# Kernel tuning notes

Measured on AMD Instinct MI355X. Metric: run time of the kernel, lower is better.

The kernel has to match this reference:

```python
import jax, jax.numpy as jnp
import numpy as np
from math import sqrt

ROPE_BASE = 6000.0


def _rope_tables(seq_len, rope_dim, dtype):
    # inv_freq: [rope_dim/2]; emb = concat(freqs, freqs) along last dim -> [seq_len, rope_dim]
    inv_freq = 1.0 / (ROPE_BASE ** (jnp.arange(0, rope_dim, 2, dtype=jnp.float32) / rope_dim))
    t = jnp.arange(seq_len, dtype=jnp.float32)
    freqs = jnp.outer(t, inv_freq)
    emb = jnp.concatenate([freqs, freqs], axis=-1)
    return jnp.cos(emb).astype(dtype), jnp.sin(emb).astype(dtype)


def _rotate_half(x):
    x1, x2 = jnp.split(x, 2, axis=-1)
    return jnp.concatenate([-x2, x1], axis=-1)


def setup_inputs() -> dict:
    key = jax.random.key(0)
    k1, k2, k3 = jax.random.split(key, 3)
    B, S, D = 2, 2048, 1024
    H, DK = 16, 64
    x = jax.random.normal(k1, (B, S, D), dtype=jnp.float32)
    W_qkv = jax.random.normal(k2, (3, H, DK, D), dtype=jnp.float32) * 0.02
    W_o = jax.random.normal(k3, (D, H * DK), dtype=jnp.float32) * 0.02
    return {"x": x, "W_qkv": W_qkv, "W_o": W_o}


def reference(x, W_qkv, W_o):
    B, S, D = x.shape
    _, H, DK, _ = W_qkv.shape
    rope_dim = DK // 2  # RotaryEmbeddings(dim=d_k // 2)

    # fused QKV projection: [B, 3, H, S, DK]
    qkv = jnp.einsum('bsm,qhdm->bqhsd', x, W_qkv)

    # inline RoPE on Q and K, first rope_dim channels only
    cos, sin = _rope_tables(S, rope_dim, x.dtype)  # [S, rope_dim]
    qk = qkv[:, :2, :, :, :rope_dim]
    qk_rot = qk * cos + _rotate_half(qk) * sin
    qkv = qkv.at[:, :2, :, :, :rope_dim].set(qk_rot)

    Q, K, V = qkv[:, 0], qkv[:, 1], qkv[:, 2]  # [B, H, S, DK]

    scores = jnp.einsum('bhqd,bhkd->bhqk', Q, K)
    causal = jnp.triu(jnp.ones((S, S), dtype=bool), k=1)
    scores = jnp.where(causal, -jnp.inf, scores) / sqrt(DK)
    attn = jax.nn.softmax(scores, axis=-1)
    out = jnp.einsum('bhqk,bhkd->bhqd', attn, V)

    # concat heads: [B, S, H*DK], then output projection (Linear weight [D, H*DK])
    out = out.transpose(0, 2, 1, 3).reshape(B, S, H * DK)
    return jnp.einsum('bsh,dh->bsd', out, W_o)
```

## Files before the change

kernel.cpp:

```cpp
#include <hip/hip_runtime.h>
#include <math.h>


static constexpr int Bb  = 2;
static constexpr int Ss  = 2048;
static constexpr int Hh  = 16;
static constexpr int DKk = 64;

static constexpr size_t QSZ = (size_t)Bb * Hh * Ss * DKk;

static constexpr size_t WOB_E  = 0;
static constexpr size_t XB_E   = 1048576;
static constexpr size_t WQKV_E = 5242880;
static constexpr size_t QB_E   = 9437184;
static constexpr size_t OB_E   = QB_E + 3*QSZ;

typedef __attribute__((ext_vector_type(8))) short short8;
typedef __attribute__((ext_vector_type(4))) float f32x4;

__device__ __forceinline__ unsigned short f2bf(float f) {
    unsigned int u = __float_as_uint(f);
    u += 0x7fffu + ((u >> 16) & 1u);
    return (unsigned short)(u >> 16);
}

__device__ __forceinline__ unsigned int cvtpk_bf16(float lo, float hi) {
    unsigned int r;
    asm("v_cvt_pk_bf16_f32 %0, %1, %2" : "=v"(r) : "v"(lo), "v"(hi));
    return r;
}

__device__ __forceinline__ float fexp2(float x) {
    float r;
    asm("v_exp_f32 %0, %1" : "=v"(r) : "v"(x));
    return r;
}

__device__ __forceinline__ float fsin_rev(float r) {
    float o;
    asm("v_sin_f32 %0, %1" : "=v"(o) : "v"(r));
    return o;
}
__device__ __forceinline__ float fcos_rev(float r) {
    float o;
    asm("v_cos_f32 %0, %1" : "=v"(o) : "v"(r));
    return o;
}

__device__ __forceinline__ void gl16(const unsigned short* g, unsigned short* l) {
    __builtin_amdgcn_global_load_lds(
        (const __attribute__((address_space(1))) void*)g,
        (__attribute__((address_space(3))) void*)l, 16, 0, 0);
}

__global__ __launch_bounds__(256)
void convert_bf16(const float* __restrict__ x, const float* __restrict__ wqkv,
                  const float* __restrict__ wo, unsigned short* __restrict__ dst)
{
    const size_t i4 = ((size_t)blockIdx.x * 256 + threadIdx.x) * 4;
    const float* src;
    if (i4 < 1048576)      src = wo   + i4;
    else if (i4 < 5242880) src = x    + (i4 - 1048576);
    else                   src = wqkv + (i4 - 5242880);
    const float4 v = *(const float4*)src;
    ushort4 p = { f2bf(v.x), f2bf(v.y), f2bf(v.z), f2bf(v.w) };
    *(ushort4*)(dst + i4) = p;
}

template<int MODE, int BN>
__global__ __launch_bounds__(256)
void gemm_mfma(const unsigned short* __restrict__ A,
               const unsigned short* __restrict__ Bm,
               float* __restrict__ C, unsigned short* __restrict__ QKV, int N)
{
    constexpr int K   = 1024;
    constexpr int NF  = BN / 32;
    constexpr int ASZ = 128 * 32;
    constexpr int BSZ = BN * 32;
    __shared__ unsigned short ShPool[2 * ASZ + 2 * BSZ];
    unsigned short* As0 = ShPool;
    unsigned short* As1 = ShPool + ASZ;
    unsigned short* Bs0 = ShPool + 2 * ASZ;
    unsigned short* Bs1 = ShPool + 2 * ASZ + BSZ;

    const int t    = threadIdx.x;
    const int lane = t & 63;
    const int w    = t >> 6;
    const int l15  = lane & 15;
    const int quad = lane >> 4;
    const int wr   = w >> 1;
    const int wc   = w & 1;
    const int n0   = blockIdx.x * BN;
    const int m0   = blockIdx.y * 128;

    const unsigned short* Ag = A  + (size_t)(m0 + (t >> 2)) * K + (t & 3) * 8;
    const unsigned short* Bg = Bm + (size_t)(n0 + (t >> 2)) * K + (t & 3) * 8;

    f32x4 acc[4][NF];
    #pragma unroll
    for (int i = 0; i < 4; i++)
        #pragma unroll
        for (int j = 0; j < NF; j++) acc[i][j] = f32x4{0.f, 0.f, 0.f, 0.f};

    auto stage = [&](int k0, unsigned short* Asb, unsigned short* Bsb) {
        gl16(Ag + k0,        Asb + t*8);
        gl16(Ag + 64*K + k0, Asb + 2048 + t*8);
        gl16(Bg + k0,        Bsb + t*8);
        if (BN == 128) gl16(Bg + 64*K + k0, Bsb + 2048 + t*8);
    };
    auto comp = [&](const unsigned short* Asb, const unsigned short* Bsb) {
        short8 af[4], bfv[NF];
        #pragma unroll
        for (int mf = 0; mf < 4; mf++)
            af[mf] = *(const short8*)&Asb[(wr*64 + mf*16 + l15) * 32 + quad*8];
        #pragma unroll
        for (int nf = 0; nf < NF; nf++)
            bfv[nf] = *(const short8*)&Bsb[(wc*(BN/2) + nf*16 + l15) * 32 + quad*8];
        #pragma unroll
        for (int mf = 0; mf < 4; mf++)
            #pragma unroll
            for (int nf = 0; nf < NF; nf++)
                acc[mf][nf] = __builtin_amdgcn_mfma_f32_16x16x32_bf16(
                    af[mf], bfv[nf], acc[mf][nf], 0, 0, 0);
    };

    stage(0, As0, Bs0);
    for (int k0 = 0; k0 < K; k0 += 64) {
        __syncthreads();
        stage(k0 + 32, As1, Bs1);
        comp(As0, Bs0);
        __syncthreads();
        if (k0 + 64 < K) stage(k0 + 64, As0, Bs0);
        comp(As1, Bs1);
    }

    if (MODE == 0) {
        #pragma unroll
        for (int mf = 0; mf < 4; mf++)
            #pragma unroll
            for (int r = 0; r < 4; r++) {
                float* crow = C + (size_t)(m0 + wr*64 + mf*16 + quad*4 + r) * N
                            + n0 + wc*(BN/2);
                #pragma unroll
                for (int nf = 0; nf < NF; nf++)
                    crow[nf*16 + l15] = acc[mf][nf][r];
            }
    } else {
        __syncthreads();
        const int col0 = n0 + wc*64;
        const int q    = col0 >> 10;
        const int h    = (col0 >> 6) & 15;
        const int row0 = m0 + wr*64;
        const int b    = row0 >> 11;
        const int s0   = row0 & 2047;
        if (q == 2) {
            unsigned short* chunk = ShPool + w * 2048;
            unsigned short* vb = QKV + 2*QSZ
                               + (size_t)(b*Hh + h) * DKk * Ss + s0;
            #pragma unroll
            for (int pass = 0; pass < 2; pass++) {
                #pragma unroll
                for (int mf = 0; mf < 4; mf++)
                    #pragma unroll
                    for (int nfp = 0; nfp < 2; nfp++) {
                        const int nf = pass*2 + nfp;
                        const int dl = nfp*16 + l15;
                        const int sby = (mf*16 + quad*4) * 2;
                        ushort4 pv = { f2bf(acc[mf][nf][0]), f2bf(acc[mf][nf][1]),
                                       f2bf(acc[mf][nf][2]), f2bf(acc[mf][nf][3]) };
                        *(ushort4*)((char*)chunk
                            + dl*128 + (sby ^ ((dl & 7) << 4))) = pv;
                    }
                #pragma unroll
                for (int dblk = 0; dblk < 8; dblk++) {
                    const int dl = dblk*4 + quad;
                    const int sl = l15*4;
                    const ushort4 pv = *(const ushort4*)((char*)chunk
                        + dl*128 + ((sl*2) ^ ((dl & 7) << 4)));
                    *(ushort4*)(vb + (size_t)(pass*32 + dl) * Ss + sl) = pv;
                }
            }
        } else {
            const float qsc = (q == 0) ? 0.125f * 1.44269504088896f : 1.0f;
            const float rev_freq = (float)(exp(-(double)(2 * l15) / 32.0
                                   * log(6000.0)) / 6.283185307179586);
            unsigned short* base = QKV + (size_t)q * QSZ
                                 + ((size_t)(b*Hh + h) * Ss) * DKk;
            #pragma unroll
            for (int mf = 0; mf < 4; mf++)
                #pragma unroll
                for (int r = 0; r < 4; r++) {
                    const int s = s0 + mf*16 + quad*4 + r;
                    float rev = (float)s * rev_freq;
                    rev -= floorf(rev);
                    const float sn = fsin_rev(rev);
                    const float cs = fcos_rev(rev);
                    const float v0 = acc[mf][0][r] * qsc;
                    const float v1 = acc[mf][1][r] * qsc;
                    unsigned short* rowp = base + (size_t)s * DKk;
                    rowp[l15]      = f2bf(v0 * cs - v1 * sn);
                    rowp[16 + l15] = f2bf(v1 * cs + v0 * sn);
                    rowp[32 + l15] = f2bf(acc[mf][2][r] * qsc);
                    rowp[48 + l15] = f2bf(acc[mf][3][r] * qsc);
                }
        }
    }
}

__global__ __launch_bounds__(256)
void flash_mfma(const unsigned short* __restrict__ Qa,
                const unsigned short* __restrict__ Ka,
                const unsigned short* __restrict__ Va,
                unsigned short* __restrict__ Ob)
{
    __shared__ unsigned short Ks0[64*64];
    __shared__ unsigned short Ks1[64*64];
    __shared__ unsigned short Vs0[64*64];
    __shared__ unsigned short Vs1[64*64];

    const int t    = threadIdx.x;
    const int lane = t & 63;
    const int w    = t >> 6;
    const int l15  = lane & 15;
    const int quad = lane >> 4;

    const int bid   = blockIdx.x;
    const int xcd   = bid & 7;
    const int slot  = bid >> 3;
    const bool hv   = slot < 32;
    const int sub   = hv ? slot : slot - 32;
    const int bh    = xcd*4 + (sub >> 3);
    const int j     = sub & 7;
    const int QT    = hv ? 15 - j : j;
    const int n     = 2*QT + 2;

    const int c0 = t,       r0 = c0 >> 3, g0 = ((c0 & 7) ^ (r0 & 7)) * 8;
    const int c1 = t + 256, r1 = c1 >> 3, g1 = ((c1 & 7) ^ (r1 & 7)) * 8;

    auto stage = [&](int skt, unsigned short* Ksb, unsigned short* Vsb) {
        const unsigned short* Kg = Ka + (size_t)bh * Ss * DKk + (size_t)skt*64*DKk;
        const unsigned short* Vg = Va + (size_t)bh * DKk * Ss + skt*64;
        gl16(Kg + (size_t)r0*DKk + g0, Ksb + t*8);
        gl16(Kg + (size_t)r1*DKk + g1, Ksb + (t+256)*8);
        gl16(Vg + (size_t)r0*Ss  + g0, Vsb + t*8);
        gl16(Vg + (size_t)r1*Ss  + g1, Vsb + (t+256)*8);
    };

    short8 qf[2][2];
    f32x4 o[2][4];
    float lacc[2];
    #pragma unroll
    for (int mfq = 0; mfq < 2; mfq++) {
        lacc[mfq] = 0.f;
        #pragma unroll
        for (int i = 0; i < 4; i++) o[mfq][i] = f32x4{0.f,0.f,0.f,0.f};
    }
    #pragma unroll
    for (int mfq = 0; mfq < 2; mfq++) {
        const unsigned short* qrow = Qa + (size_t)bh * Ss * DKk
            + (size_t)(QT*128 + w*32 + mfq*16 + l15) * DKk;
        qf[mfq][0] = *(const short8*)(qrow + quad*8);
        qf[mfq][1] = *(const short8*)(qrow + 32 + quad*8);
    }

    auto compute = [&](const unsigned short* Ksb, const unsigned short* Vsb,
                       int ckt) {
        f32x4 sc[4][2];
        #pragma unroll
        for (int nt = 0; nt < 4; nt++)
            #pragma unroll
            for (int mfq = 0; mfq < 2; mfq++) sc[nt][mfq] = f32x4{0.f,0.f,0.f,0.f};
        #pragma unroll
        for (int nt = 0; nt < 4; nt++)
            #pragma unroll
            for (int kc = 0; kc < 2; kc++) {
                const short8 kf = *(const short8*)&Ksb[(nt*16 + l15)*64
                                   + (((kc*4 + quad) ^ (l15 & 7)) * 8)];
                sc[nt][0] = __builtin_amdgcn_mfma_f32_16x16x32_bf16(kf, qf[0][kc], sc[nt][0], 0,0,0);
                sc[nt][1] = __builtin_amdgcn_mfma_f32_16x16x32_bf16(kf, qf[1][kc], sc[nt][1], 0,0,0);
            }

        if (ckt >= 2*QT) {
            const int kb = ckt*64 + quad*4;
            const int qb = QT*128 + w*32 + l15;
            #pragma unroll
            for (int nt = 0; nt < 4; nt++)
                #pragma unroll
                for (int mfq = 0; mfq < 2; mfq++)
                    #pragma unroll
                    for (int r = 0; r < 4; r++)
                        if (kb + nt*16 + r > qb + mfq*16)
                            sc[nt][mfq][r] = -INFINITY;
        }

        #pragma unroll
        for (int nt = 0; nt < 4; nt++)
            #pragma unroll
            for (int mfq = 0; mfq < 2; mfq++)
                #pragma unroll
                for (int r = 0; r < 4; r++)
                    sc[nt][mfq][r] = fexp2(sc[nt][mfq][r]);
        #pragma unroll
        for (int mfq = 0; mfq < 2; mfq++)
            #pragma unroll
            for (int nt = 0; nt < 4; nt++)
                lacc[mfq] += (sc[nt][mfq][0] + sc[nt][mfq][1])
                           + (sc[nt][mfq][2] + sc[nt][mfq][3]);

        short8 pfrag[2][2];
        #pragma unroll
        for (int mfq = 0; mfq < 2; mfq++)
            #pragma unroll
            for (int kc = 0; kc < 2; kc++) {
                unsigned int pk[4];
                #pragma unroll
                for (int v = 0; v < 4; v++) {
                    const int nt = 2*kc + (v >> 1);
                    const int rr = 2*(v & 1);
                    pk[v] = cvtpk_bf16(sc[nt][mfq][rr], sc[nt][mfq][rr+1]);
                }
                pfrag[mfq][kc] = *(short8*)&pk[0];
            }

        #pragma unroll
        for (int dt = 0; dt < 4; dt++) {
            const int row = dt*16 + l15;
            const int rx  = row & 7;
            const int wi  = 4*(quad & 1);
            #pragma unroll
            for (int kc = 0; kc < 2; kc++) {
                const ushort4 lo = *(const ushort4*)&Vsb[row*64
                                    + (((4*kc + (quad>>1)) ^ rx) * 8) + wi];
                const ushort4 hi = *(const ushort4*)&Vsb[row*64
                                    + (((4*kc + 2 + (quad>>1)) ^ rx) * 8) + wi];
                short8 vf;
                vf[0]=lo.x; vf[1]=lo.y; vf[2]=lo.z; vf[3]=lo.w;
                vf[4]=hi.x; vf[5]=hi.y; vf[6]=hi.z; vf[7]=hi.w;
                o[0][dt] = __builtin_amdgcn_mfma_f32_16x16x32_bf16(
                    pfrag[0][kc], vf, o[0][dt], 0,0,0);
                o[1][dt] = __builtin_amdgcn_mfma_f32_16x16x32_bf16(
                    pfrag[1][kc], vf, o[1][dt], 0,0,0);
            }
        }
    };

    stage(0, Ks0, Vs0);
    int i = 0;
    while (true) {
        __syncthreads();
        const bool h1 = (i + 1 < n);
        if (h1) stage(i + 1, Ks1, Vs1);
        compute(Ks0, Vs0, i);
        if (!h1) break;
        i++;
        __syncthreads();
        const bool h2 = (i + 1 < n);
        if (h2) stage(i + 1, Ks0, Vs0);
        compute(Ks1, Vs1, i);
        if (!h2) break;
        i++;
    }

    {
        const int b = bh >> 4, h = bh & 15;
        const int q0 = QT*128 + w*32;
        #pragma unroll
        for (int mfq = 0; mfq < 2; mfq++) {
            float ls = lacc[mfq];
            ls += __shfl_xor(ls, 16);
            ls += __shfl_xor(ls, 32);
            #pragma unroll
            for (int r = 0; r < 4; r++) {
                const int x = quad*4 + r;
                const float inv = 1.0f / __shfl(ls, (lane & 48) + x);
                const int row = q0 + mfq*16 + x;
                unsigned short* orow = Ob + ((size_t)b*Ss + row) * 1024 + h*64;
                #pragma unroll
                for (int dt = 0; dt < 4; dt++)
                    orow[dt*16 + l15] = f2bf(o[mfq][dt][r] * inv);
            }
        }
    }
}

extern "C" void kernel_launch(void* const* d_in, const int* in_sizes, int n_in,
                              void* d_out, int out_size, void* d_ws, size_t ws_size,
                              hipStream_t stream)
{
    const float* x    = (const float*)d_in[0];
    const float* Wqkv = (const float*)d_in[1];
    const float* Wo   = (const float*)d_in[2];
    float* out = (float*)d_out;
    unsigned short* wsu = (unsigned short*)d_ws;

    const dim3 blk(256);
    convert_bf16<<<dim3(8192), blk, 0, stream>>>(x, Wqkv, Wo, wsu);
    gemm_mfma<1,128><<<dim3(24, 32), blk, 0, stream>>>(wsu + XB_E, wsu + WQKV_E,
                                                       nullptr, wsu + QB_E, 3072);
    flash_mfma<<<dim3(512), blk, 0, stream>>>(wsu + QB_E, wsu + QB_E + QSZ,
                                              wsu + QB_E + 2*QSZ, wsu + OB_E);
    gemm_mfma<0,64><<<dim3(16, 32), blk, 0, stream>>>(wsu + OB_E, wsu + WOB_E,
                                                      out, nullptr, 1024);
}
```

Baseline: 171.0 us.

## Double the flash-attention KV tile to 128 keys and raise MFMA wave priority

The key/value tile staged per iteration grows from 64 to 128 keys. This halves the number of loop iterations and barriers, and the causal mask only needs to be applied on the diagonal tile. V shared-memory rows widen to 128 with a 16-way XOR swizzle, and the score and P fragment arrays double in size. s_setprio calls bracket the MFMA sections so waves in matrix math are scheduled ahead of others. In exchange, LDS use doubles to 64KB per block and register pressure rises, which may lower occupancy.

```diff
diff --git a/kernel.cpp b/kernel.cpp
--- a/kernel.cpp
+++ b/kernel.cpp
@@ -213,10 +213,10 @@
                 const unsigned short* __restrict__ Va,
                 unsigned short* __restrict__ Ob)
 {
-    __shared__ unsigned short Ks0[64*64];
-    __shared__ unsigned short Ks1[64*64];
-    __shared__ unsigned short Vs0[64*64];
-    __shared__ unsigned short Vs1[64*64];
+    __shared__ unsigned short Ks0[128*64];
+    __shared__ unsigned short Ks1[128*64];
+    __shared__ unsigned short Vs0[64*128];
+    __shared__ unsigned short Vs1[64*128];
 
     const int t    = threadIdx.x;
     const int lane = t & 63;
@@ -232,18 +232,24 @@
     const int bh    = xcd*4 + (sub >> 3);
     const int j     = sub & 7;
     const int QT    = hv ? 15 - j : j;
-    const int n     = 2*QT + 2;
-
-    const int c0 = t,       r0 = c0 >> 3, g0 = ((c0 & 7) ^ (r0 & 7)) * 8;
-    const int c1 = t + 256, r1 = c1 >> 3, g1 = ((c1 & 7) ^ (r1 & 7)) * 8;
+    const int n     = QT + 1;
+
+    int rK[4], gK[4], rV[4], gV[4];
+    #pragma unroll
+    for (int i = 0; i < 4; i++) {
+        const int c = t + 256*i;
+        rK[i] = c >> 3;  gK[i] = ((c & 7)  ^ (rK[i] & 7))  * 8;
+        rV[i] = c >> 4;  gV[i] = ((c & 15) ^ (rV[i] & 15)) * 8;
+    }
 
     auto stage = [&](int skt, unsigned short* Ksb, unsigned short* Vsb) {
-        const unsigned short* Kg = Ka + (size_t)bh * Ss * DKk + (size_t)skt*64*DKk;
-        const unsigned short* Vg = Va + (size_t)bh * DKk * Ss + skt*64;
-        gl16(Kg + (size_t)r0*DKk + g0, Ksb + t*8);
-        gl16(Kg + (size_t)r1*DKk + g1, Ksb + (t+256)*8);
-        gl16(Vg + (size_t)r0*Ss  + g0, Vsb + t*8);
-        gl16(Vg + (size_t)r1*Ss  + g1, Vsb + (t+256)*8);
+        const unsigned short* Kg = Ka + (size_t)bh * Ss * DKk + (size_t)skt*128*DKk;
+        const unsigned short* Vg = Va + (size_t)bh * DKk * Ss + skt*128;
+        #pragma unroll
+        for (int i = 0; i < 4; i++) {
+            gl16(Kg + (size_t)rK[i]*DKk + gK[i], Ksb + (t + 256*i)*8);
+            gl16(Vg + (size_t)rV[i]*Ss  + gV[i], Vsb + (t + 256*i)*8);
+        }
     };
 
     short8 qf[2][2];
@@ -265,13 +271,14 @@
 
     auto compute = [&](const unsigned short* Ksb, const unsigned short* Vsb,
                        int ckt) {
-        f32x4 sc[4][2];
-        #pragma unroll
-        for (int nt = 0; nt < 4; nt++)
+        f32x4 sc[8][2];
+        #pragma unroll
+        for (int nt = 0; nt < 8; nt++)
             #pragma unroll
             for (int mfq = 0; mfq < 2; mfq++) sc[nt][mfq] = f32x4{0.f,0.f,0.f,0.f};
-        #pragma unroll
-        for (int nt = 0; nt < 4; nt++)
+        __builtin_amdgcn_s_setprio(1);
+        #pragma unroll
+        for (int nt = 0; nt < 8; nt++)
             #pragma unroll
             for (int kc = 0; kc < 2; kc++) {
                 const short8 kf = *(const short8*)&Ksb[(nt*16 + l15)*64
@@ -279,12 +286,13 @@
                 sc[nt][0] = __builtin_amdgcn_mfma_f32_16x16x32_bf16(kf, qf[0][kc], sc[nt][0], 0,0,0);
                 sc[nt][1] = __builtin_amdgcn_mfma_f32_16x16x32_bf16(kf, qf[1][kc], sc[nt][1], 0,0,0);
             }
-
-        if (ckt >= 2*QT) {
-            const int kb = ckt*64 + quad*4;
-            const int qb = QT*128 + w*32 + l15;
-            #pragma unroll
-            for (int nt = 0; nt < 4; nt++)
+        __builtin_amdgcn_s_setprio(0);
+
+        if (ckt == QT) {
+            const int kb = quad*4;
+            const int qb = w*32 + l15;
+            #pragma unroll
+            for (int nt = 0; nt < 8; nt++)
                 #pragma unroll
                 for (int mfq = 0; mfq < 2; mfq++)
                     #pragma unroll
@@ -294,7 +302,7 @@
         }
 
         #pragma unroll
-        for (int nt = 0; nt < 4; nt++)
+        for (int nt = 0; nt < 8; nt++)
             #pragma unroll
             for (int mfq = 0; mfq < 2; mfq++)
                 #pragma unroll
@@ -303,15 +311,15 @@
         #pragma unroll
         for (int mfq = 0; mfq < 2; mfq++)
             #pragma unroll
-            for (int nt = 0; nt < 4; nt++)
+            for (int nt = 0; nt < 8; nt++)
                 lacc[mfq] += (sc[nt][mfq][0] + sc[nt][mfq][1])
                            + (sc[nt][mfq][2] + sc[nt][mfq][3]);
 
-        short8 pfrag[2][2];
+        short8 pfrag[2][4];
         #pragma unroll
         for (int mfq = 0; mfq < 2; mfq++)
             #pragma unroll
-            for (int kc = 0; kc < 2; kc++) {
+            for (int kc = 0; kc < 4; kc++) {
                 unsigned int pk[4];
                 #pragma unroll
                 for (int v = 0; v < 4; v++) {
@@ -322,16 +330,17 @@
                 pfrag[mfq][kc] = *(short8*)&pk[0];
             }
 
+        __builtin_amdgcn_s_setprio(1);
         #pragma unroll
         for (int dt = 0; dt < 4; dt++) {
             const int row = dt*16 + l15;
-            const int rx  = row & 7;
+            const int rx  = row & 15;
             const int wi  = 4*(quad & 1);
             #pragma unroll
-            for (int kc = 0; kc < 2; kc++) {
-                const ushort4 lo = *(const ushort4*)&Vsb[row*64
+            for (int kc = 0; kc < 4; kc++) {
+                const ushort4 lo = *(const ushort4*)&Vsb[row*128
                                     + (((4*kc + (quad>>1)) ^ rx) * 8) + wi];
-                const ushort4 hi = *(const ushort4*)&Vsb[row*64
+                const ushort4 hi = *(const ushort4*)&Vsb[row*128
                                     + (((4*kc + 2 + (quad>>1)) ^ rx) * 8) + wi];
                 short8 vf;
                 vf[0]=lo.x; vf[1]=lo.y; vf[2]=lo.z; vf[3]=lo.w;
@@ -342,6 +351,7 @@
                     pfrag[1][kc], vf, o[1][dt], 0,0,0);
             }
         }
+        __builtin_amdgcn_s_setprio(0);
     };
 
     stage(0, Ks0, Vs0);
```

New measurement: 187.9 us. +9.9%, slower.

## Retile GEMMs to smaller blocks with row-split warps for more CTAs

Applied to the files above, without the earlier changes.

The GEMM template gains a BM parameter, and each of the four waves now owns a horizontal strip of rows across the full BN columns instead of a 2x2 warp grid. The QKV projection uses 128x64 tiles (1536 blocks), and the output projection uses 64x64 tiles (1024 blocks), giving more blocks to fill the GPU. The V transpose epilogue is rewritten to stage the whole tile in shared memory and write it back in one cooperative pass. Smaller tiles lower per-block data reuse and add global traffic, and each wave now reloads all of the B fragments.

```diff
diff --git a/kernel.cpp b/kernel.cpp
--- a/kernel.cpp
+++ b/kernel.cpp
@@ -67,59 +67,60 @@
     *(ushort4*)(dst + i4) = p;
 }
 
-template<int MODE, int BN>
+template<int MODE, int BM, int BN>
 __global__ __launch_bounds__(256)
 void gemm_mfma(const unsigned short* __restrict__ A,
                const unsigned short* __restrict__ Bm,
                float* __restrict__ C, unsigned short* __restrict__ QKV, int N)
 {
     constexpr int K   = 1024;
-    constexpr int NF  = BN / 32;
-    constexpr int ASZ = 128 * 32;
+    constexpr int MF  = BM / 64;
+    constexpr int NFr = BN / 16;
+    constexpr int ASZ = BM * 32;
     constexpr int BSZ = BN * 32;
-    __shared__ unsigned short ShPool[2 * ASZ + 2 * BSZ];
+    __shared__ unsigned short ShPool[2*ASZ + 2*BSZ];
     unsigned short* As0 = ShPool;
     unsigned short* As1 = ShPool + ASZ;
-    unsigned short* Bs0 = ShPool + 2 * ASZ;
-    unsigned short* Bs1 = ShPool + 2 * ASZ + BSZ;
+    unsigned short* Bs0 = ShPool + 2*ASZ;
+    unsigned short* Bs1 = ShPool + 2*ASZ + BSZ;
 
     const int t    = threadIdx.x;
     const int lane = t & 63;
     const int w    = t >> 6;
     const int l15  = lane & 15;
     const int quad = lane >> 4;
-    const int wr   = w >> 1;
-    const int wc   = w & 1;
     const int n0   = blockIdx.x * BN;
-    const int m0   = blockIdx.y * 128;
+    const int m0   = blockIdx.y * BM;
 
     const unsigned short* Ag = A  + (size_t)(m0 + (t >> 2)) * K + (t & 3) * 8;
     const unsigned short* Bg = Bm + (size_t)(n0 + (t >> 2)) * K + (t & 3) * 8;
 
-    f32x4 acc[4][NF];
+    f32x4 acc[MF][NFr];
     #pragma unroll
-    for (int i = 0; i < 4; i++)
-        #pragma unroll
-        for (int j = 0; j < NF; j++) acc[i][j] = f32x4{0.f, 0.f, 0.f, 0.f};
+    for (int i = 0; i < MF; i++)
+        #pragma unroll
+        for (int j = 0; j < NFr; j++) acc[i][j] = f32x4{0.f, 0.f, 0.f, 0.f};
 
     auto stage = [&](int k0, unsigned short* Asb, unsigned short* Bsb) {
-        gl16(Ag + k0,        Asb + t*8);
-        gl16(Ag + 64*K + k0, Asb + 2048 + t*8);
-        gl16(Bg + k0,        Bsb + t*8);
-        if (BN == 128) gl16(Bg + 64*K + k0, Bsb + 2048 + t*8);
+        #pragma unroll
+        for (int rr = 0; rr < BM/64; rr++)
+            gl16(Ag + (size_t)rr*64*K + k0, Asb + rr*2048 + t*8);
+        #pragma unroll
+        for (int rr = 0; rr < BN/64; rr++)
+            gl16(Bg + (size_t)rr*64*K + k0, Bsb + rr*2048 + t*8);
     };
     auto comp = [&](const unsigned short* Asb, const unsigned short* Bsb) {
-        short8 af[4], bfv[NF];
-        #pragma unroll
-        for (int mf = 0; mf < 4; mf++)
-            af[mf] = *(const short8*)&Asb[(wr*64 + mf*16 + l15) * 32 + quad*8];
-        #pragma unroll
-        for (int nf = 0; nf < NF; nf++)
-            bfv[nf] = *(const short8*)&Bsb[(wc*(BN/2) + nf*16 + l15) * 32 + quad*8];
-        #pragma unroll
-        for (int mf = 0; mf < 4; mf++)
-            #pragma unroll
-            for (int nf = 0; nf < NF; nf++)
+        short8 af[MF], bfv[NFr];
+        #pragma unroll
+        for (int mf = 0; mf < MF; mf++)
+            af[mf] = *(const short8*)&Asb[(w*(BM/4) + mf*16 + l15) * 32 + quad*8];
+        #pragma unroll
+        for (int nf = 0; nf < NFr; nf++)
+            bfv[nf] = *(const short8*)&Bsb[(nf*16 + l15) * 32 + quad*8];
+        #pragma unroll
+        for (int mf = 0; mf < MF; mf++)
+            #pragma unroll
+            for (int nf = 0; nf < NFr; nf++)
                 acc[mf][nf] = __builtin_amdgcn_mfma_f32_16x16x32_bf16(
                     af[mf], bfv[nf], acc[mf][nf], 0, 0, 0);
     };
@@ -136,49 +137,43 @@
 
     if (MODE == 0) {
         #pragma unroll
-        for (int mf = 0; mf < 4; mf++)
+        for (int mf = 0; mf < MF; mf++)
             #pragma unroll
             for (int r = 0; r < 4; r++) {
-                float* crow = C + (size_t)(m0 + wr*64 + mf*16 + quad*4 + r) * N
-                            + n0 + wc*(BN/2);
-                #pragma unroll
-                for (int nf = 0; nf < NF; nf++)
+                float* crow = C + (size_t)(m0 + w*(BM/4) + mf*16 + quad*4 + r) * N
+                            + n0;
+                #pragma unroll
+                for (int nf = 0; nf < NFr; nf++)
                     crow[nf*16 + l15] = acc[mf][nf][r];
             }
     } else {
         __syncthreads();
-        const int col0 = n0 + wc*64;
-        const int q    = col0 >> 10;
-        const int h    = (col0 >> 6) & 15;
-        const int row0 = m0 + wr*64;
-        const int b    = row0 >> 11;
-        const int s0   = row0 & 2047;
+        const int q  = n0 >> 10;
+        const int h  = (n0 >> 6) & 15;
+        const int b  = m0 >> 11;
+        const int s0 = m0 & 2047;
         if (q == 2) {
-            unsigned short* chunk = ShPool + w * 2048;
+            #pragma unroll
+            for (int mf = 0; mf < MF; mf++)
+                #pragma unroll
+                for (int nf = 0; nf < NFr; nf++) {
+                    const int d  = nf*16 + l15;
+                    const int sl = w*(BM/4) + mf*16 + quad*4;
+                    ushort4 pv = { f2bf(acc[mf][nf][0]), f2bf(acc[mf][nf][1]),
+                                   f2bf(acc[mf][nf][2]), f2bf(acc[mf][nf][3]) };
+                    *(ushort4*)((char*)ShPool
+                        + d*256 + ((sl*2) ^ ((d & 15) << 4))) = pv;
+                }
+            __syncthreads();
             unsigned short* vb = QKV + 2*QSZ
                                + (size_t)(b*Hh + h) * DKk * Ss + s0;
             #pragma unroll
-            for (int pass = 0; pass < 2; pass++) {
-                #pragma unroll
-                for (int mf = 0; mf < 4; mf++)
-                    #pragma unroll
-                    for (int nfp = 0; nfp < 2; nfp++) {
-                        const int nf = pass*2 + nfp;
-                        const int dl = nfp*16 + l15;
-                        const int sby = (mf*16 + quad*4) * 2;
-                        ushort4 pv = { f2bf(acc[mf][nf][0]), f2bf(acc[mf][nf][1]),
-                                       f2bf(acc[mf][nf][2]), f2bf(acc[mf][nf][3]) };
-                        *(ushort4*)((char*)chunk
-                            + dl*128 + (sby ^ ((dl & 7) << 4))) = pv;
-                    }
-                #pragma unroll
-                for (int dblk = 0; dblk < 8; dblk++) {
-                    const int dl = dblk*4 + quad;
-                    const int sl = l15*4;
-                    const ushort4 pv = *(const ushort4*)((char*)chunk
-                        + dl*128 + ((sl*2) ^ ((dl & 7) << 4)));
-                    *(ushort4*)(vb + (size_t)(pass*32 + dl) * Ss + sl) = pv;
-                }
+            for (int p = 0; p < 8; p++) {
+                const int d  = p*8 + (t >> 5);
+                const int s4 = (t & 31) * 4;
+                const ushort4 pv = *(const ushort4*)((char*)ShPool
+                    + d*256 + ((s4*2) ^ ((d & 15) << 4)));
+                *(ushort4*)(vb + (size_t)d * Ss + s4) = pv;
             }
         } else {
             const float qsc = (q == 0) ? 0.125f * 1.44269504088896f : 1.0f;
@@ -187,10 +182,10 @@
             unsigned short* base = QKV + (size_t)q * QSZ
                                  + ((size_t)(b*Hh + h) * Ss) * DKk;
             #pragma unroll
-            for (int mf = 0; mf < 4; mf++)
+            for (int mf = 0; mf < MF; mf++)
                 #pragma unroll
                 for (int r = 0; r < 4; r++) {
-                    const int s = s0 + mf*16 + quad*4 + r;
+                    const int s = s0 + w*(BM/4) + mf*16 + quad*4 + r;
                     float rev = (float)s * rev_freq;
                     rev -= floorf(rev);
                     const float sn = fsin_rev(rev);
@@ -395,10 +390,10 @@
 
     const dim3 blk(256);
     convert_bf16<<<dim3(8192), blk, 0, stream>>>(x, Wqkv, Wo, wsu);
-    gemm_mfma<1,128><<<dim3(24, 32), blk, 0, stream>>>(wsu + XB_E, wsu + WQKV_E,
-                                                       nullptr, wsu + QB_E, 3072);
+    gemm_mfma<1,128,64><<<dim3(48, 32), blk, 0, stream>>>(wsu + XB_E,
+                                    wsu + WQKV_E, nullptr, wsu + QB_E, 3072);
     flash_mfma<<<dim3(512), blk, 0, stream>>>(wsu + QB_E, wsu + QB_E + QSZ,
                                               wsu + QB_E + 2*QSZ, wsu + OB_E);
-    gemm_mfma<0,64><<<dim3(16, 32), blk, 0, stream>>>(wsu + OB_E, wsu + WOB_E,
-                                                      out, nullptr, 1024);
-}
+    gemm_mfma<0,64,64><<<dim3(16, 64), blk, 0, stream>>>(wsu + OB_E,
+                                    wsu + WOB_E, out, nullptr, 1024);
+}
```

Measured after the change: 174.5 us. 2.0% more time.
